# Optimization experiments

Measured on AMD Instinct MI355X. Metric: run time of the kernel, lower is better.

Reference implementation:

```python
import jax, jax.numpy as jnp
import numpy as np

# Config (matches init_kwargs)
N, A, H, W = 4, 16, 384, 384
B_SIZE = 8      # block_size per spatial dim
STRIDE = 4      # block_stride per spatial dim (overlapping blocks)
THRESH = 2.0    # singular-value soft threshold
NB = (H - B_SIZE) // STRIDE + 1   # blocks per spatial dim (95)
P = B_SIZE * B_SIZE               # pixels per block (64)


def _block_indices():
    """Flat pixel index for each (block, in-block pixel): [NB*NB, P] int32."""
    starts = np.arange(NB) * STRIDE
    ih = starts[:, None] + np.arange(B_SIZE)              # [NB, b] row coords
    flat = ih[:, None, :, None] * W + ih[None, :, None, :]  # [NBh, NBw, b, b]
    return flat.reshape(NB * NB, P).astype(np.int32)


def setup_inputs() -> dict:
    key = jax.random.key(0)
    x = jax.random.normal(key, (N, A, H, W), dtype=jnp.float32)
    idx = jnp.asarray(_block_indices())
    # precompute_normalization: overlap-add of ones -> per-pixel block count
    block_weights = jnp.zeros(H * W, jnp.float32).at[idx].add(1.0).reshape(H, W)
    return {"x": x, "block_weights": block_weights}


def reference(x, block_weights):
    idx = jnp.asarray(_block_indices())           # [B, P]
    # self.shift = (0, 0) on the first forward call -> rolls are identity
    x = jnp.roll(x, (0, 0), axis=(-2, -1))
    xf = x.reshape(N, A, H * W)
    blocks = xf[:, :, idx]                        # [N, A, B, P] block extraction
    m = jnp.transpose(blocks, (0, 2, 3, 1))       # 'n a b p -> n b p a' -> [N,B,P,A]
    U, S, Vh = jnp.linalg.svd(m, full_matrices=False)  # U:[N,B,P,A] S:[N,B,A] Vh:[N,B,A,A]
    S = jnp.maximum(S - THRESH, 0.0)              # soft-threshold singular values
    m = (U * S[..., None, :]) @ Vh                # U diag(S) Vh, [N,B,P,A]
    blocks = jnp.transpose(m, (0, 3, 1, 2))       # 'n b p a -> n a b p'
    # adjoint: overlap-add fold, then normalize by block counts
    out = jnp.zeros((N, A, H * W), x.dtype).at[:, :, idx].add(blocks)
    out = out.reshape(N, A, H, W) / block_weights
    return jnp.roll(out, (0, 0), axis=(-2, -1))
```

## Files before the change

kernel.cpp:

```cpp
#include <hip/hip_runtime.h>


typedef __attribute__((ext_vector_type(2))) float v2f;
typedef union { float4 f4; v2f v2[2]; } f4v2;

#define N_      4
#define A_      16
#define H_      384
#define W_      384
#define PLANE_  (H_*W_)
#define NB_     95
#define NBB_    (NB_*NB_)
#define NMAT_   (N_*NBB_)
#define NWAVE_  ((NMAT_ + 3) / 4)
#define NSWEEP_ 4
#define PHI_BYTES_ ((size_t)NMAT_ * 256 * 4)

template<int CTRL>
__device__ __forceinline__ float dpp16(float v) {
    union { float f; int i; } u; u.f = v;
    u.i = __builtin_amdgcn_mov_dpp(u.i, CTRL, 0xF, 0xF, true);
    return u.f;
}

#define QP1_ 0xB1
#define QP2_ 0x4E
#define QP3_ 0x1B
#define HM_  0x141
#define FM_  0x140
#define R8_  0x128

template<int M>
__device__ __forceinline__ float lane_xor16(float v) {
    if constexpr (M == 1)       return dpp16<QP1_>(v);
    else if constexpr (M == 2)  return dpp16<QP2_>(v);
    else if constexpr (M == 3)  return dpp16<QP3_>(v);
    else if constexpr (M == 7)  return dpp16<HM_>(v);
    else if constexpr (M == 8)  return dpp16<R8_>(v);
    else if constexpr (M == 15) return dpp16<FM_>(v);
    else if constexpr (M == 4)  return dpp16<QP3_>(dpp16<HM_>(v));
    else if constexpr (M == 5)  return dpp16<QP2_>(dpp16<HM_>(v));
    else if constexpr (M == 6)  return dpp16<QP1_>(dpp16<HM_>(v));
    else if constexpr (M == 9)  return dpp16<QP1_>(dpp16<R8_>(v));
    else if constexpr (M == 10) return dpp16<QP2_>(dpp16<R8_>(v));
    else if constexpr (M == 11) return dpp16<QP3_>(dpp16<R8_>(v));
    else if constexpr (M == 12) return dpp16<QP3_>(dpp16<FM_>(v));
    else if constexpr (M == 13) return dpp16<QP2_>(dpp16<FM_>(v));
    else                        return dpp16<QP1_>(dpp16<FM_>(v));
}

template<int M>
__device__ __forceinline__ void jacobi_round(v2f w[8], float& nrm, const int j) {
    v2f pw[8];
    #pragma unroll
    for (int i = 0; i < 8; ++i) {
        pw[i][0] = lane_xor16<M>(w[i][0]);
        pw[i][1] = lane_xor16<M>(w[i][1]);
    }
    const float pn = lane_xor16<M>(nrm);

    v2f d0 = w[0]*pw[0], d1 = w[1]*pw[1];
    #pragma unroll
    for (int i = 2; i < 8; i += 2) {
        d0 = __builtin_elementwise_fma(w[i],   pw[i],   d0);
        d1 = __builtin_elementwise_fma(w[i+1], pw[i+1], d1);
    }
    const v2f dsum = d0 + d1;
    const float gam = dsum[0] + dsum[1];

    const bool  low = ((j ^ M) > j);
    const float na  = low ? nrm : pn;
    const float nb  = low ? pn  : nrm;

    const float thr = 1e-12f * (na + nb);
    const bool  rot = fabsf(gam) > thr;
    const float gs  = rot ? gam : 1.f;
    const float zeta = (nb - na) * (0.5f * __builtin_amdgcn_rcpf(gs));
    const float rt   = __builtin_amdgcn_rcpf(
                           fabsf(zeta) +
                           __builtin_amdgcn_sqrtf(__builtin_fmaf(zeta, zeta, 1.f)));
    float t  = copysignf(rt, zeta);
    float c  = __builtin_amdgcn_rsqf(__builtin_fmaf(t, t, 1.f));
    float sv = c * t;
    if (!rot) { c = 1.f; sv = 0.f; }

    const float ss = low ? -sv : sv;
    const v2f c2 = {c, c}, sp = {ss, ss};
    #pragma unroll
    for (int i = 0; i < 8; ++i)
        w[i] = __builtin_elementwise_fma(c2, w[i], sp*pw[i]);

    const float cc = c*c, s2 = sv*sv, x2 = 2.f*c*sv*gam;
    nrm = low ? (cc*na + s2*nb - x2) : (s2*na + cc*nb + x2);
}

__device__ __forceinline__ void gram_jacobi_phi(
        const float* __restrict__ x, const int wid, const int warp,
        const int lane, float Gl[4][4][320]) {
    const int g   = lane >> 4;
    const int j   = lane & 15;
    const int kq4 = g * 4;
    float* const mt = &Gl[warp][3][0];

    for (int s = 0; s < 4; ++s) {
        const int id  = wid * 4 + s;
        const int n   = id / NBB_;
        const int rem = id % NBB_;
        const int bi  = rem / NB_;
        const int bj  = rem % NB_;
        const int pbase = n * (A_ * PLANE_) + bi*4*W_ + bj*4;

        v2f acc0 = {0,0}, acc1 = {0,0}, acc2 = {0,0}, acc3 = {0,0};
        for (int q = 0; q < 4; ++q) {
            const int p    = q*16 + j;
            const int base = pbase + (p >> 3) * W_ + (p & 7);
            __builtin_amdgcn_wave_barrier();
            #pragma unroll
            for (int t = 0; t < 4; ++t)
                mt[(kq4 + t)*20 + j] = x[base + (kq4 + t) * PLANE_];
            __builtin_amdgcn_wave_barrier();

            #pragma unroll
            for (int p4 = 0; p4 < 16; p4 += 4) {
                f4v2 av, b0, b1, b2, b3;
                av.f4 = *(const float4*)&mt[j*20 + p4];
                b0.f4 = *(const float4*)&mt[(kq4 + 0)*20 + p4];
                b1.f4 = *(const float4*)&mt[(kq4 + 1)*20 + p4];
                b2.f4 = *(const float4*)&mt[(kq4 + 2)*20 + p4];
                b3.f4 = *(const float4*)&mt[(kq4 + 3)*20 + p4];
                #pragma unroll
                for (int h = 0; h < 2; ++h) {
                    acc0 = __builtin_elementwise_fma(av.v2[h], b0.v2[h], acc0);
                    acc1 = __builtin_elementwise_fma(av.v2[h], b1.v2[h], acc1);
                    acc2 = __builtin_elementwise_fma(av.v2[h], b2.v2[h], acc2);
                    acc3 = __builtin_elementwise_fma(av.v2[h], b3.v2[h], acc3);
                }
            }
            __builtin_amdgcn_wave_barrier();
        }
        *(float4*)&Gl[warp][s][j*20 + kq4] =
            make_float4(acc0[0]+acc0[1], acc1[0]+acc1[1],
                        acc2[0]+acc2[1], acc3[0]+acc3[1]);
    }
    __builtin_amdgcn_wave_barrier();

    v2f w[8];
    {
        f4v2 t0, t1, t2, t3;
        t0.f4 = *(const float4*)&Gl[warp][g][j*20 + 0];
        t1.f4 = *(const float4*)&Gl[warp][g][j*20 + 4];
        t2.f4 = *(const float4*)&Gl[warp][g][j*20 + 8];
        t3.f4 = *(const float4*)&Gl[warp][g][j*20 + 12];
        w[0]=t0.v2[0]; w[1]=t0.v2[1]; w[2]=t1.v2[0]; w[3]=t1.v2[1];
        w[4]=t2.v2[0]; w[5]=t2.v2[1]; w[6]=t3.v2[0]; w[7]=t3.v2[1];
    }
    float nrm;
    {
        v2f d = w[0]*w[0];
        #pragma unroll
        for (int i = 1; i < 8; ++i) d = __builtin_elementwise_fma(w[i], w[i], d);
        nrm = d[0] + d[1];
    }

    for (int sweep = 0; sweep < NSWEEP_; ++sweep) {
        jacobi_round<1>(w, nrm, j);  jacobi_round<2>(w, nrm, j);
        jacobi_round<3>(w, nrm, j);  jacobi_round<4>(w, nrm, j);
        jacobi_round<5>(w, nrm, j);  jacobi_round<6>(w, nrm, j);
        jacobi_round<7>(w, nrm, j);  jacobi_round<8>(w, nrm, j);
        jacobi_round<9>(w, nrm, j);  jacobi_round<10>(w, nrm, j);
        jacobi_round<11>(w, nrm, j); jacobi_round<12>(w, nrm, j);
        jacobi_round<13>(w, nrm, j); jacobi_round<14>(w, nrm, j);
        jacobi_round<15>(w, nrm, j);
    }
    {
        v2f d = w[0]*w[0];
        #pragma unroll
        for (int i = 1; i < 8; ++i) d = __builtin_elementwise_fma(w[i], w[i], d);
        nrm = d[0] + d[1];
    }
    float rho = 0.f;
    if (nrm > 16.f) {
        const float lam = __builtin_amdgcn_sqrtf(nrm);
        rho = (1.f - 2.f * __builtin_amdgcn_rsqf(lam)) * __builtin_amdgcn_rcpf(nrm);
    }

    __builtin_amdgcn_wave_barrier();
    *(float4*)&Gl[warp][g][j*20 + 0]  = make_float4(w[0][0], w[0][1], w[1][0], w[1][1]);
    *(float4*)&Gl[warp][g][j*20 + 4]  = make_float4(w[2][0], w[2][1], w[3][0], w[3][1]);
    *(float4*)&Gl[warp][g][j*20 + 8]  = make_float4(w[4][0], w[4][1], w[5][0], w[5][1]);
    *(float4*)&Gl[warp][g][j*20 + 12] = make_float4(w[6][0], w[6][1], w[7][0], w[7][1]);
    Gl[warp][g][j*20 + 16] = rho;
    __builtin_amdgcn_wave_barrier();

    v2f ph[8];
    #pragma unroll
    for (int i = 0; i < 8; ++i) ph[i] = (v2f){0.f, 0.f};
    #pragma unroll
    for (int k = 0; k < 16; ++k) {
        const float coef = Gl[warp][g][k*20 + 16] * Gl[warp][g][k*20 + j];
        const v2f cf = {coef, coef};
        f4v2 c0, c1, c2r, c3;
        c0.f4  = *(const float4*)&Gl[warp][g][k*20 + 0];
        c1.f4  = *(const float4*)&Gl[warp][g][k*20 + 4];
        c2r.f4 = *(const float4*)&Gl[warp][g][k*20 + 8];
        c3.f4  = *(const float4*)&Gl[warp][g][k*20 + 12];
        ph[0] = __builtin_elementwise_fma(cf, c0.v2[0],  ph[0]);
        ph[1] = __builtin_elementwise_fma(cf, c0.v2[1],  ph[1]);
        ph[2] = __builtin_elementwise_fma(cf, c1.v2[0],  ph[2]);
        ph[3] = __builtin_elementwise_fma(cf, c1.v2[1],  ph[3]);
        ph[4] = __builtin_elementwise_fma(cf, c2r.v2[0], ph[4]);
        ph[5] = __builtin_elementwise_fma(cf, c2r.v2[1], ph[5]);
        ph[6] = __builtin_elementwise_fma(cf, c3.v2[0],  ph[6]);
        ph[7] = __builtin_elementwise_fma(cf, c3.v2[1],  ph[7]);
    }
    __builtin_amdgcn_wave_barrier();
    *(float4*)&Gl[warp][g][j*20 + 0]  = make_float4(ph[0][0], ph[0][1], ph[1][0], ph[1][1]);
    *(float4*)&Gl[warp][g][j*20 + 4]  = make_float4(ph[2][0], ph[2][1], ph[3][0], ph[3][1]);
    *(float4*)&Gl[warp][g][j*20 + 8]  = make_float4(ph[4][0], ph[4][1], ph[5][0], ph[5][1]);
    *(float4*)&Gl[warp][g][j*20 + 12] = make_float4(ph[6][0], ph[6][1], ph[7][0], ph[7][1]);
    __builtin_amdgcn_wave_barrier();
}

__global__ __launch_bounds__(256, 8)
void llr_phi(const float* __restrict__ x, float* __restrict__ phiG) {
    __shared__ __align__(16) float Gl[4][4][320];
    const int warp = threadIdx.x >> 6;
    const int lane = threadIdx.x & 63;

    const int xcd = blockIdx.x & 7, idx = blockIdx.x >> 3;
    const int wg  = (xcd == 0 ? idx : 283 + (xcd - 1) * 282 + idx);
    const int wid = wg * 4 + warp;
    if (wid >= NWAVE_) return;

    gram_jacobi_phi(x, wid, warp, lane, Gl);

    const int g = lane >> 4, j = lane & 15;
    float* pb = phiG + (size_t)(wid*4 + g) * 256 + j * 16;
    const float4 p0 = *(const float4*)&Gl[warp][g][j*20 + 0];
    const float4 p1 = *(const float4*)&Gl[warp][g][j*20 + 4];
    const float4 p2 = *(const float4*)&Gl[warp][g][j*20 + 8];
    const float4 p3 = *(const float4*)&Gl[warp][g][j*20 + 12];
    *(float4*)&pb[0]  = p0;  *(float4*)&pb[4]  = p1;
    *(float4*)&pb[8]  = p2;  *(float4*)&pb[12] = p3;
}

__global__ __launch_bounds__(256, 8)
void llr_out2(const float* __restrict__ x, const float* __restrict__ phiG,
              float* __restrict__ out) {
    __shared__ __align__(16) float Sl[16][260];

    const int b  = (blockIdx.x & 7) * 288 + (blockIdx.x >> 3);
    const int n  = b / 576;
    const int tt = b % 576;
    const int tr = tt / 12, tc = tt % 12;
    const int r0 = tr*8, c0 = tc*32;
    const int cr0 = tr*2, cc0 = tc*8;

    {
        const int lc = threadIdx.x >> 4;
        const int fo = (threadIdx.x & 15) * 4;
        const int ci = cr0 + (lc >> 3);
        const int cj = cc0 + (lc & 7);
        const int bi0 = max(ci - 1, 0), bi1 = min(ci, NB_ - 1);
        const int bj0 = max(cj - 1, 0), bj1 = min(cj, NB_ - 1);
        const size_t r00 = ((size_t)(n*NBB_ + bi0*NB_ + bj0))*256;
        const size_t r01 = ((size_t)(n*NBB_ + bi0*NB_ + bj1))*256;
        const size_t r10 = ((size_t)(n*NBB_ + bi1*NB_ + bj0))*256;
        const size_t r11 = ((size_t)(n*NBB_ + bi1*NB_ + bj1))*256;
        #pragma unroll
        for (int it = 0; it < 4; ++it) {
            const int off = fo + it*64;
            const float4 a  = *(const float4*)&phiG[r00 + off];
            const float4 bq = *(const float4*)&phiG[r01 + off];
            const float4 cq = *(const float4*)&phiG[r10 + off];
            const float4 d  = *(const float4*)&phiG[r11 + off];
            float4 s;
            s.x = (a.x + bq.x + cq.x + d.x) * 0.25f;
            s.y = (a.y + bq.y + cq.y + d.y) * 0.25f;
            s.z = (a.z + bq.z + cq.z + d.z) * 0.25f;
            s.w = (a.w + bq.w + cq.w + d.w) * 0.25f;
            *(float4*)&Sl[lc][off] = s;
        }
    }
    __syncthreads();

    const int r = threadIdx.x >> 5;
    const int c = threadIdx.x & 31;
    const int lcc = ((r >> 2) << 3) + (c >> 2);
    const size_t sb = (size_t)n * (A_*PLANE_) + (size_t)(r0 + r) * W_ + (c0 + c);

    float xk[16];
    #pragma unroll
    for (int k = 0; k < 16; ++k) xk[k] = x[sb + (size_t)k * PLANE_];

    v2f acc[8];
    #pragma unroll
    for (int i = 0; i < 8; ++i) acc[i] = (v2f){0.f, 0.f};
    #pragma unroll
    for (int k = 0; k < 16; ++k) {
        const v2f xv = {xk[k], xk[k]};
        f4v2 s0, s1, s2, s3;
        s0.f4 = *(const float4*)&Sl[lcc][k*16 + 0];
        s1.f4 = *(const float4*)&Sl[lcc][k*16 + 4];
        s2.f4 = *(const float4*)&Sl[lcc][k*16 + 8];
        s3.f4 = *(const float4*)&Sl[lcc][k*16 + 12];
        acc[0] = __builtin_elementwise_fma(xv, s0.v2[0], acc[0]);
        acc[1] = __builtin_elementwise_fma(xv, s0.v2[1], acc[1]);
        acc[2] = __builtin_elementwise_fma(xv, s1.v2[0], acc[2]);
        acc[3] = __builtin_elementwise_fma(xv, s1.v2[1], acc[3]);
        acc[4] = __builtin_elementwise_fma(xv, s2.v2[0], acc[4]);
        acc[5] = __builtin_elementwise_fma(xv, s2.v2[1], acc[5]);
        acc[6] = __builtin_elementwise_fma(xv, s3.v2[0], acc[6]);
        acc[7] = __builtin_elementwise_fma(xv, s3.v2[1], acc[7]);
    }
    #pragma unroll
    for (int i = 0; i < 8; ++i) {
        out[sb + (size_t)(2*i)     * PLANE_] = acc[i][0];
        out[sb + (size_t)(2*i + 1) * PLANE_] = acc[i][1];
    }
}

__global__ __launch_bounds__(256, 5)
void llr_fused(const float* __restrict__ x, float* __restrict__ out) {
    __shared__ __align__(16) float Gl[4][4][320];
    const int warp = threadIdx.x >> 6;
    const int lane = threadIdx.x & 63;
    const int wid  = blockIdx.x * 4 + warp;
    if (wid >= NWAVE_) return;

    gram_jacobi_phi(x, wid, warp, lane, Gl);

    const int pr = lane >> 3, pc = lane & 7;
    for (int s = 0; s < 4; ++s) {
        const int id = wid*4 + s;
        const int n = id / NBB_, rem = id % NBB_;
        const int bi = rem / NB_, bj = rem % NB_;
        const int base = n*(A_*PLANE_) + (bi*4+pr)*W_ + (bj*4+pc);
        float mr[16];
        #pragma unroll
        for (int a = 0; a < 16; ++a) mr[a] = x[base + a*PLANE_];
        float o[16];
        #pragma unroll
        for (int a = 0; a < 16; ++a) o[a] = 0.f;
        #pragma unroll
        for (int k = 0; k < 16; ++k) {
            const float mk = mr[k];
            const float4 f0 = *(const float4*)&Gl[warp][s][k*20 + 0];
            const float4 f1 = *(const float4*)&Gl[warp][s][k*20 + 4];
            const float4 f2 = *(const float4*)&Gl[warp][s][k*20 + 8];
            const float4 f3 = *(const float4*)&Gl[warp][s][k*20 + 12];
            o[0]+=mk*f0.x;  o[1]+=mk*f0.y;  o[2]+=mk*f0.z;  o[3]+=mk*f0.w;
            o[4]+=mk*f1.x;  o[5]+=mk*f1.y;  o[6]+=mk*f1.z;  o[7]+=mk*f1.w;
            o[8]+=mk*f2.x;  o[9]+=mk*f2.y;  o[10]+=mk*f2.z; o[11]+=mk*f2.w;
            o[12]+=mk*f3.x; o[13]+=mk*f3.y; o[14]+=mk*f3.z; o[15]+=mk*f3.w;
        }
        #pragma unroll
        for (int a = 0; a < 16; ++a)
            unsafeAtomicAdd(&out[base + a*PLANE_], o[a]);
    }
}

__global__ __launch_bounds__(256)
void llr_div(float* __restrict__ out, const float* __restrict__ bw) {
    const int i = (blockIdx.x * 256 + threadIdx.x) * 4;
    float4 o = *(float4*)&out[i];
    const float4 bv = *(const float4*)&bw[i % PLANE_];
    o.x /= bv.x; o.y /= bv.y; o.z /= bv.z; o.w /= bv.w;
    *(float4*)&out[i] = o;
}

extern "C" void kernel_launch(void* const* d_in, const int* in_sizes, int n_in,
                              void* d_out, int out_size, void* d_ws, size_t ws_size,
                              hipStream_t stream) {
    (void)in_sizes; (void)n_in;
    const float* x  = (const float*)d_in[0];
    const float* bw = (const float*)d_in[1];
    float* out = (float*)d_out;

    if (ws_size >= PHI_BYTES_) {
        float* phiG = (float*)d_ws;
        hipLaunchKernelGGL(llr_phi,  dim3((NWAVE_ + 3) / 4), dim3(256), 0, stream, x, phiG);
        hipLaunchKernelGGL(llr_out2, dim3(4 * 48 * 12),      dim3(256), 0, stream, x, phiG, out);
    } else {
        hipMemsetAsync(out, 0, (size_t)out_size * sizeof(float), stream);
        hipLaunchKernelGGL(llr_fused, dim3((NWAVE_ + 3) / 4), dim3(256), 0, stream, x, out);
        hipLaunchKernelGGL(llr_div, dim3((N_*A_*PLANE_) / (256*4)), dim3(256), 0, stream, out, bw);
    }
}
```

Before: 201.4 us.

## Prefetch block tiles with float4 loads, force packed FMA, simplify Jacobi norm update

Block loading in the Gram stage moves from scalar per-lane gathers to four float4 row loads per lane, and the next block's tiles are prefetched into registers while the current block's Gram product is computed. All elementwise v2f FMAs are forced to v_pk_fma/v_pk_mul/v_pk_add through inline asm so the compiler cannot split them into scalar ops. The Jacobi column-norm update becomes the closed form nrm ± t*gam instead of recomputing from c and s. These target global-load latency and VALU instruction count, at the cost of extra prefetch registers, possibly lower occupancy, and a small numerical change in the norm update.

```diff
diff --git a/kernel.cpp b/kernel.cpp
--- a/kernel.cpp
+++ b/kernel.cpp
@@ -15,6 +15,19 @@
 #define NWAVE_  ((NMAT_ + 3) / 4)
 #define NSWEEP_ 4
 #define PHI_BYTES_ ((size_t)NMAT_ * 256 * 4)
+
+__device__ __forceinline__ v2f pk_fma(v2f a, v2f b, v2f c) {
+    v2f d; asm("v_pk_fma_f32 %0, %1, %2, %3" : "=v"(d) : "v"(a), "v"(b), "v"(c));
+    return d;
+}
+__device__ __forceinline__ v2f pk_mul(v2f a, v2f b) {
+    v2f d; asm("v_pk_mul_f32 %0, %1, %2" : "=v"(d) : "v"(a), "v"(b));
+    return d;
+}
+__device__ __forceinline__ v2f pk_add(v2f a, v2f b) {
+    v2f d; asm("v_pk_add_f32 %0, %1, %2" : "=v"(d) : "v"(a), "v"(b));
+    return d;
+}
 
 template<int CTRL>
 __device__ __forceinline__ float dpp16(float v) {
@@ -59,14 +72,14 @@
     }
     const float pn = lane_xor16<M>(nrm);
 
-    v2f d0 = w[0]*pw[0], d1 = w[1]*pw[1];
+    v2f d0 = pk_mul(w[0], pw[0]), d1 = pk_mul(w[1], pw[1]);
     #pragma unroll
     for (int i = 2; i < 8; i += 2) {
-        d0 = __builtin_elementwise_fma(w[i],   pw[i],   d0);
-        d1 = __builtin_elementwise_fma(w[i+1], pw[i+1], d1);
-    }
-    const v2f dsum = d0 + d1;
-    const float gam = dsum[0] + dsum[1];
+        d0 = pk_fma(w[i],   pw[i],   d0);
+        d1 = pk_fma(w[i+1], pw[i+1], d1);
+    }
+    const v2f ds = pk_add(d0, d1);
+    const float gam = ds[0] + ds[1];
 
     const bool  low = ((j ^ M) > j);
     const float na  = low ? nrm : pn;
@@ -82,16 +95,15 @@
     float t  = copysignf(rt, zeta);
     float c  = __builtin_amdgcn_rsqf(__builtin_fmaf(t, t, 1.f));
     float sv = c * t;
-    if (!rot) { c = 1.f; sv = 0.f; }
+    if (!rot) { c = 1.f; sv = 0.f; t = 0.f; }
 
     const float ss = low ? -sv : sv;
     const v2f c2 = {c, c}, sp = {ss, ss};
     #pragma unroll
     for (int i = 0; i < 8; ++i)
-        w[i] = __builtin_elementwise_fma(c2, w[i], sp*pw[i]);
-
-    const float cc = c*c, s2 = sv*sv, x2 = 2.f*c*sv*gam;
-    nrm = low ? (cc*na + s2*nb - x2) : (s2*na + cc*nb + x2);
+        w[i] = pk_fma(c2, w[i], pk_mul(sp, pw[i]));
+
+    nrm = __builtin_fmaf(low ? -t : t, gam, nrm);
 }
 
 __device__ __forceinline__ void gram_jacobi_phi(
@@ -100,24 +112,43 @@
     const int g   = lane >> 4;
     const int j   = lane & 15;
     const int kq4 = g * 4;
+    const int cst = lane & 15;
+    const int rh  = lane >> 4;
     float* const mt = &Gl[warp][3][0];
 
-    for (int s = 0; s < 4; ++s) {
+    auto sbase = [&](int s) -> const float* {
         const int id  = wid * 4 + s;
         const int n   = id / NBB_;
         const int rem = id % NBB_;
         const int bi  = rem / NB_;
         const int bj  = rem % NB_;
-        const int pbase = n * (A_ * PLANE_) + bi*4*W_ + bj*4;
+        return x + n * (A_ * PLANE_) + bi*4*W_ + bj*4
+                 + cst * PLANE_ + (rh >> 1) * W_ + (rh & 1) * 4;
+    };
+
+    const float* p0 = sbase(0);
+    float4 va = *(const float4*)(p0);
+    float4 vb = *(const float4*)(p0 + 2*W_);
+    float4 vc = *(const float4*)(p0 + 4*W_);
+    float4 vd = *(const float4*)(p0 + 6*W_);
+
+    #pragma unroll
+    for (int s = 0; s < 4; ++s) {
+        float4 na_, nb_, nc_, nd_;
+        if (s < 3) {
+            const float* pn_ = sbase(s + 1);
+            na_ = *(const float4*)(pn_);
+            nb_ = *(const float4*)(pn_ + 2*W_);
+            nc_ = *(const float4*)(pn_ + 4*W_);
+            nd_ = *(const float4*)(pn_ + 6*W_);
+        }
 
         v2f acc0 = {0,0}, acc1 = {0,0}, acc2 = {0,0}, acc3 = {0,0};
+        #pragma unroll
         for (int q = 0; q < 4; ++q) {
-            const int p    = q*16 + j;
-            const int base = pbase + (p >> 3) * W_ + (p & 7);
             __builtin_amdgcn_wave_barrier();
-            #pragma unroll
-            for (int t = 0; t < 4; ++t)
-                mt[(kq4 + t)*20 + j] = x[base + (kq4 + t) * PLANE_];
+            const float4 vq = (q == 0) ? va : (q == 1) ? vb : (q == 2) ? vc : vd;
+            *(float4*)&mt[cst*20 + rh*4] = vq;
             __builtin_amdgcn_wave_barrier();
 
             #pragma unroll
@@ -130,10 +161,10 @@
                 b3.f4 = *(const float4*)&mt[(kq4 + 3)*20 + p4];
                 #pragma unroll
                 for (int h = 0; h < 2; ++h) {
-                    acc0 = __builtin_elementwise_fma(av.v2[h], b0.v2[h], acc0);
-                    acc1 = __builtin_elementwise_fma(av.v2[h], b1.v2[h], acc1);
-                    acc2 = __builtin_elementwise_fma(av.v2[h], b2.v2[h], acc2);
-                    acc3 = __builtin_elementwise_fma(av.v2[h], b3.v2[h], acc3);
+                    acc0 = pk_fma(av.v2[h], b0.v2[h], acc0);
+                    acc1 = pk_fma(av.v2[h], b1.v2[h], acc1);
+                    acc2 = pk_fma(av.v2[h], b2.v2[h], acc2);
+                    acc3 = pk_fma(av.v2[h], b3.v2[h], acc3);
                 }
             }
             __builtin_amdgcn_wave_barrier();
@@ -141,6 +172,7 @@
         *(float4*)&Gl[warp][s][j*20 + kq4] =
             make_float4(acc0[0]+acc0[1], acc1[0]+acc1[1],
                         acc2[0]+acc2[1], acc3[0]+acc3[1]);
+        if (s < 3) { va = na_; vb = nb_; vc = nc_; vd = nd_; }
     }
     __builtin_amdgcn_wave_barrier();
 
@@ -156,9 +188,9 @@
     }
     float nrm;
     {
-        v2f d = w[0]*w[0];
-        #pragma unroll
-        for (int i = 1; i < 8; ++i) d = __builtin_elementwise_fma(w[i], w[i], d);
+        v2f d = pk_mul(w[0], w[0]);
+        #pragma unroll
+        for (int i = 1; i < 8; ++i) d = pk_fma(w[i], w[i], d);
         nrm = d[0] + d[1];
     }
 
@@ -173,9 +205,9 @@
         jacobi_round<15>(w, nrm, j);
     }
     {
-        v2f d = w[0]*w[0];
-        #pragma unroll
-        for (int i = 1; i < 8; ++i) d = __builtin_elementwise_fma(w[i], w[i], d);
+        v2f d = pk_mul(w[0], w[0]);
+        #pragma unroll
+        for (int i = 1; i < 8; ++i) d = pk_fma(w[i], w[i], d);
         nrm = d[0] + d[1];
     }
     float rho = 0.f;
@@ -204,14 +236,14 @@
         c1.f4  = *(const float4*)&Gl[warp][g][k*20 + 4];
         c2r.f4 = *(const float4*)&Gl[warp][g][k*20 + 8];
         c3.f4  = *(const float4*)&Gl[warp][g][k*20 + 12];
-        ph[0] = __builtin_elementwise_fma(cf, c0.v2[0],  ph[0]);
-        ph[1] = __builtin_elementwise_fma(cf, c0.v2[1],  ph[1]);
-        ph[2] = __builtin_elementwise_fma(cf, c1.v2[0],  ph[2]);
-        ph[3] = __builtin_elementwise_fma(cf, c1.v2[1],  ph[3]);
-        ph[4] = __builtin_elementwise_fma(cf, c2r.v2[0], ph[4]);
-        ph[5] = __builtin_elementwise_fma(cf, c2r.v2[1], ph[5]);
-        ph[6] = __builtin_elementwise_fma(cf, c3.v2[0],  ph[6]);
-        ph[7] = __builtin_elementwise_fma(cf, c3.v2[1],  ph[7]);
+        ph[0] = pk_fma(cf, c0.v2[0],  ph[0]);
+        ph[1] = pk_fma(cf, c0.v2[1],  ph[1]);
+        ph[2] = pk_fma(cf, c1.v2[0],  ph[2]);
+        ph[3] = pk_fma(cf, c1.v2[1],  ph[3]);
+        ph[4] = pk_fma(cf, c2r.v2[0], ph[4]);
+        ph[5] = pk_fma(cf, c2r.v2[1], ph[5]);
+        ph[6] = pk_fma(cf, c3.v2[0],  ph[6]);
+        ph[7] = pk_fma(cf, c3.v2[1],  ph[7]);
     }
     __builtin_amdgcn_wave_barrier();
     *(float4*)&Gl[warp][g][j*20 + 0]  = make_float4(ph[0][0], ph[0][1], ph[1][0], ph[1][1]);
@@ -304,14 +336,14 @@
         s1.f4 = *(const float4*)&Sl[lcc][k*16 + 4];
         s2.f4 = *(const float4*)&Sl[lcc][k*16 + 8];
         s3.f4 = *(const float4*)&Sl[lcc][k*16 + 12];
-        acc[0] = __builtin_elementwise_fma(xv, s0.v2[0], acc[0]);
-        acc[1] = __builtin_elementwise_fma(xv, s0.v2[1], acc[1]);
-        acc[2] = __builtin_elementwise_fma(xv, s1.v2[0], acc[2]);
-        acc[3] = __builtin_elementwise_fma(xv, s1.v2[1], acc[3]);
-        acc[4] = __builtin_elementwise_fma(xv, s2.v2[0], acc[4]);
-        acc[5] = __builtin_elementwise_fma(xv, s2.v2[1], acc[5]);
-        acc[6] = __builtin_elementwise_fma(xv, s3.v2[0], acc[6]);
-        acc[7] = __builtin_elementwise_fma(xv, s3.v2[1], acc[7]);
+        acc[0] = pk_fma(xv, s0.v2[0], acc[0]);
+        acc[1] = pk_fma(xv, s0.v2[1], acc[1]);
+        acc[2] = pk_fma(xv, s1.v2[0], acc[2]);
+        acc[3] = pk_fma(xv, s1.v2[1], acc[3]);
+        acc[4] = pk_fma(xv, s2.v2[0], acc[4]);
+        acc[5] = pk_fma(xv, s2.v2[1], acc[5]);
+        acc[6] = pk_fma(xv, s3.v2[0], acc[6]);
+        acc[7] = pk_fma(xv, s3.v2[1], acc[7]);
     }
     #pragma unroll
     for (int i = 0; i < 8; ++i) {
```

Result: no change. 198.9 us (-1.2%).
